# Kernel optimization log

Measured on AMD Instinct MI355X. Metric: run time of the kernel, lower is better.

Reference implementation:

```python
import jax, jax.numpy as jnp
import numpy as np
import math

LMAX = 2
MUL_IN1 = 8
C_OUT = 16
N_BASIS = 8
MAX_RADIUS = 2.0
N_NODES = 50000
N_EDGES = 1000000
EMB_DIM = 16
MAX_ATOM = 10
OUT_DIM = C_OUT * (LMAX + 1) ** 2


def _cg(j1, j2, j3, m1, m2, m3):
    # complex Clebsch-Gordan coefficient <j1 m1 j2 m2 | j3 m3> (Racah formula)
    if m1 + m2 != m3:
        return 0.0
    f = math.factorial
    pre = math.sqrt((2 * j3 + 1) * f(j3 + j1 - j2) * f(j3 - j1 + j2) * f(j1 + j2 - j3) / f(j1 + j2 + j3 + 1))
    pre *= math.sqrt(f(j3 + m3) * f(j3 - m3) * f(j1 - m1) * f(j1 + m1) * f(j2 - m2) * f(j2 + m2))
    s = 0.0
    for k in range(0, j1 + j2 - j3 + 1):
        d = [k, j1 + j2 - j3 - k, j1 - m1 - k, j2 + m2 - k, j3 - j2 + m1 + k, j3 - j1 - m2 + k]
        if min(d) < 0:
            continue
        s += (-1) ** k / (f(d[0]) * f(d[1]) * f(d[2]) * f(d[3]) * f(d[4]) * f(d[5]))
    return pre * s


def _q(l):
    # change of basis real -> complex spherical harmonics (e3nn convention)
    q = np.zeros((2 * l + 1, 2 * l + 1), dtype=complex)
    for m in range(-l, 0):
        q[l + m, l + abs(m)] = 2 ** -0.5
        q[l + m, l - abs(m)] = -1j * 2 ** -0.5
    q[l, l] = 1.0
    for m in range(1, l + 1):
        q[l + m, l + abs(m)] = (-1) ** m * 2 ** -0.5
        q[l + m, l - abs(m)] = 1j * (-1) ** m * 2 ** -0.5
    return (-1j) ** l * q


def _real_cg(l1, l2, l3):
    C = np.zeros((2 * l1 + 1, 2 * l2 + 1, 2 * l3 + 1), dtype=complex)
    for a, m1 in enumerate(range(-l1, l1 + 1)):
        for b, m2 in enumerate(range(-l2, l2 + 1)):
            for c, m3 in enumerate(range(-l3, l3 + 1)):
                C[a, b, c] = _cg(l1, l2, l3, m1, m2, m3)
    Cr = np.einsum('ai,bj,ck,abc->ijk', _q(l1), _q(l2), np.conj(_q(l3)), C)
    re, im = np.real(Cr), np.imag(Cr)
    M = re if np.abs(re).sum() >= np.abs(im).sum() else im
    return jnp.asarray(M, dtype=jnp.float32)


PATHS = [(l1, l2, l3) for l1 in range(LMAX + 1) for l2 in range(LMAX + 1) for l3 in range(LMAX + 1) if abs(l1 - l2) <= l3 <= l1 + l2]
CGS = [_real_cg(*p) for p in PATHS]
NUM_PATHS = len(PATHS)  # 15 for lmax=2, full path policy
ALPHA = {l3: 1.0 / math.sqrt(MUL_IN1 * sum(1 for p in PATHS if p[2] == l3)) for l3 in range(LMAX + 1)}


def _sh(n):
    # real spherical harmonics up to l=2, component normalization, m = -l..l
    x, y, z = n[:, 0], n[:, 1], n[:, 2]
    s3, s15, s5 = math.sqrt(3.0), math.sqrt(15.0), math.sqrt(5.0)
    Y0 = jnp.ones_like(x)[:, None]
    Y1 = s3 * jnp.stack([y, z, x], axis=-1)
    Y2 = jnp.stack([s15 * x * y, s15 * y * z, 0.5 * s5 * (3.0 * z * z - 1.0), s15 * x * z, 0.5 * s15 * (x * x - y * y)], axis=-1)
    return [Y0, Y1, Y2]


def _soft_one_hot(x):
    # e3nn soft_one_hot_linspace, basis='gaussian', cutoff=True
    v = jnp.linspace(0.0, MAX_RADIUS, N_BASIS + 2)
    step = v[1] - v[0]
    diff = (x[:, None] - v[1:-1]) / step
    return jnp.exp(-diff * diff) / 1.12


def _forward(pos, edge_shifts, cell, emb_table, mlp_w1, mlp_b1, mlp_w2, mlp_b2, fc_w1, fc_b1, fc_w2, fc_b2, fc_w3, fc_b3, tp_weights, A, batch, edge_src, edge_dst):
    edge_cells = cell[batch[edge_src]]                              # [E,3,3]
    shift = jnp.einsum('ni,nij->nj', edge_shifts, edge_cells)       # [E,3]
    edge_vec = pos[edge_dst] - pos[edge_src] + shift                # [E,3]
    edge_len = jnp.linalg.norm(edge_vec, axis=1)                    # [E]
    n = edge_vec / jnp.maximum(edge_len, 1e-8)[:, None]
    Ai = jax.nn.silu(emb_table[A] @ mlp_w1 + mlp_b1) @ mlp_w2 + mlp_b2   # [N, MUL_IN1]
    Ai_e = Ai[edge_src]                                             # [E, MUL_IN1]
    Y = _sh(n)                                                      # [[E,1],[E,3],[E,5]]
    emb = _soft_one_hot(edge_len) * (N_BASIS ** 0.5)                # [E, N_BASIS]
    h = jax.nn.silu(emb @ fc_w1 + fc_b1)
    h = jax.nn.silu(h @ fc_w2 + fc_b2)
    gates = h @ fc_w3 + fc_b3                                       # [E, NUM_PATHS]
    E = edge_src.shape[0]
    blocks = [jnp.zeros((E, C_OUT, 2 * l + 1), pos.dtype) for l in range(LMAX + 1)]
    for p, (l1, l2, l3) in enumerate(PATHS):
        # f_in[l1][e,u,m] = Ai_e[e,u]*Y[l1][e,m]; x2[l2][e,0,n] = Y[l2][e,n]; contraction separates:
        geo = jnp.einsum('em,en,mnk->ek', Y[l1], Y[l2], CGS[p])     # [E, 2*l3+1]
        chan = Ai_e @ tp_weights[p]                                 # [E, C_OUT]
        blocks[l3] = blocks[l3] + ALPHA[l3] * (gates[:, p, None, None] * chan[:, :, None] * geo[:, None, :])
    edge_feat = jnp.concatenate([b.reshape(E, -1) for b in blocks], axis=-1)  # [E, OUT_DIM]
    out = jax.ops.segment_sum(edge_feat, edge_dst, num_segments=pos.shape[0])
    avg = float(E) / float(pos.shape[0])
    return out / max(avg, 1e-8)


def setup_inputs():
    ks = jax.random.split(jax.random.key(0), 12)
    pos = jax.random.uniform(ks[0], (N_NODES, 3), dtype=jnp.float32)
    A = jax.random.randint(ks[1], (N_NODES,), 0, MAX_ATOM)
    batch = jnp.zeros((N_NODES,), dtype=jnp.int32)
    edge_src = jax.random.randint(ks[2], (N_EDGES,), 0, N_NODES)
    edge_dst = jax.random.randint(ks[3], (N_EDGES,), 0, N_NODES)
    edge_shifts = jnp.zeros((N_EDGES, 3), dtype=jnp.float32)
    cell = jnp.eye(3, dtype=jnp.float32)[None]
    emb_table = jax.random.normal(ks[4], (MAX_ATOM, EMB_DIM), jnp.float32)
    mlp_w1 = jax.random.normal(ks[5], (EMB_DIM, 64), jnp.float32) / math.sqrt(EMB_DIM)
    mlp_b1 = jnp.zeros((64,), jnp.float32)
    mlp_w2 = jax.random.normal(ks[6], (64, MUL_IN1), jnp.float32) / 8.0
    mlp_b2 = jnp.zeros((MUL_IN1,), jnp.float32)
    fc_w1 = jax.random.normal(ks[7], (N_BASIS, 64), jnp.float32) / math.sqrt(N_BASIS)
    fc_b1 = jnp.zeros((64,), jnp.float32)
    fc_w2 = jax.random.normal(ks[8], (64, 64), jnp.float32) / 8.0
    fc_b2 = jnp.zeros((64,), jnp.float32)
    fc_w3 = jax.random.normal(ks[9], (64, NUM_PATHS), jnp.float32) / 8.0
    fc_b3 = jnp.zeros((NUM_PATHS,), jnp.float32)
    tp_weights = jax.random.normal(ks[10], (NUM_PATHS, MUL_IN1, C_OUT), jnp.float32)
    return {'pos': pos, 'A': A, 'batch': batch, 'edge_src': edge_src, 'edge_dst': edge_dst, 'edge_shifts': edge_shifts, 'cell': cell, 'emb_table': emb_table, 'mlp_w1': mlp_w1, 'mlp_b1': mlp_b1, 'mlp_w2': mlp_w2, 'mlp_b2': mlp_b2, 'fc_w1': fc_w1, 'fc_b1': fc_b1, 'fc_w2': fc_w2, 'fc_b2': fc_b2, 'fc_w3': fc_w3, 'fc_b3': fc_b3, 'tp_weights': tp_weights}


def reference(pos, A, batch, edge_src, edge_dst, edge_shifts, cell, emb_table, mlp_w1, mlp_b1, mlp_w2, mlp_b2, fc_w1, fc_b1, fc_w2, fc_b2, fc_w3, fc_b3, tp_weights):
    return _forward(pos, edge_shifts, cell, emb_table, mlp_w1, mlp_b1, mlp_w2, mlp_b2, fc_w1, fc_b1, fc_w2, fc_b2, fc_w3, fc_b3, tp_weights, A, batch, edge_src, edge_dst)
```

## Files before the change

### kernel.cpp

```cpp
#include <hip/hip_runtime.h>
#include <math.h>
#include <limits.h>

#define N_NODES  50000
#define N_EDGES  1000000
#define INV_AVG  0.05f
#define DSENT    INT_MAX
#define TSIZE    8192
#define TMAX     1.7400f

constexpr int PL1[15] = {0,0,0,1,1,1,1,1,1,2,2,2,2,2,2};
constexpr int PL2[15] = {0,1,2,0,1,1,1,2,2,0,1,1,2,2,2};
constexpr int PCGOFF[16] = {0,1,10,35,44,53,80,125,170,245,270,315,390,415,490,615};
constexpr float PALPHA[15] = {
    0.20412414523193154f, 0.14433756729740643f, 0.14433756729740643f,
    0.14433756729740643f, 0.20412414523193154f, 0.14433756729740643f,
    0.14433756729740643f, 0.14433756729740643f, 0.14433756729740643f,
    0.14433756729740643f, 0.14433756729740643f, 0.14433756729740643f,
    0.20412414523193154f, 0.14433756729740643f, 0.14433756729740643f};

__device__ __constant__ int c_L1[15]   = {0,0,0,1,1,1,1,1,1,2,2,2,2,2,2};
__device__ __constant__ int c_L2[15]   = {0,1,2,0,1,1,1,2,2,0,1,1,2,2,2};
__device__ __constant__ int c_L3[15]   = {0,1,2,1,0,1,2,1,2,2,1,2,0,1,2};
__device__ __constant__ int c_CGOFF[16] = {0,1,10,35,44,53,80,125,170,245,270,315,390,415,490,615};

struct cplxd { double re, im; };

__device__ inline double factd(int n) {
    double r = 1.0;
    for (int i = 2; i <= n; ++i) r *= (double)i;
    return r;
}

__device__ double cgc(int j1, int j2, int j3, int m1, int m2, int m3) {
    if (m1 + m2 != m3) return 0.0;
    double pre = sqrt((double)(2*j3+1) * factd(j3+j1-j2) * factd(j3-j1+j2) *
                      factd(j1+j2-j3) / factd(j1+j2+j3+1));
    pre *= sqrt(factd(j3+m3)*factd(j3-m3)*factd(j1-m1)*factd(j1+m1)*
                factd(j2-m2)*factd(j2+m2));
    double s = 0.0;
    for (int k = 0; k <= j1+j2-j3; ++k) {
        int d1 = j1+j2-j3-k, d2 = j1-m1-k, d3 = j2+m2-k,
            d4 = j3-j2+m1+k, d5 = j3-j1-m2+k;
        if (d1 < 0 || d2 < 0 || d3 < 0 || d4 < 0 || d5 < 0) continue;
        double term = 1.0 / (factd(k)*factd(d1)*factd(d2)*factd(d3)*factd(d4)*factd(d5));
        s += (k & 1) ? -term : term;
    }
    return pre * s;
}

__device__ inline cplxd qent(int l, int a, int i) {
    const double r2 = 0.70710678118654752440;
    double re = 0.0, im = 0.0;
    int m = a - l;
    if (m < 0) {
        if (i == l - m)      re = r2;
        else if (i == l + m) im = -r2;
    } else if (m == 0) {
        if (i == l) re = 1.0;
    } else {
        double s = (m & 1) ? -1.0 : 1.0;
        if (i == l + m)      re = s * r2;
        else if (i == l - m) im = s * r2;
    }
    if (l == 1)      { double t = re; re = im; im = -t; }
    else if (l == 2) { re = -re; im = -im; }
    cplxd q; q.re = re; q.im = im; return q;
}

__device__ inline float silu_f(float x) { return x / (1.0f + __expf(-x)); }

__global__ __launch_bounds__(1024) void setup_kernel(
    float* __restrict__ cg_out,
    const float* __restrict__ fw1, const float* __restrict__ fb1,
    const float* __restrict__ fw2, const float* __restrict__ fb2,
    const float* __restrict__ fw3, const float* __restrict__ fb3,
    float* __restrict__ gtab,
    const int* __restrict__ A, const float* __restrict__ emb_table,
    const float* __restrict__ mw1, const float* __restrict__ mb1,
    const float* __restrict__ mw2, const float* __restrict__ mb2,
    float* __restrict__ Ai)
{
    const int blk = blockIdx.x;
    const int t = threadIdx.x;

    if (blk == 0) {
        __shared__ double s_re[615], s_im[615];
        __shared__ int s_flag[15];
        int p = 0;
        if (t < 615) {
            p = 14;
            while (t < c_CGOFF[p]) --p;
            int l1 = c_L1[p], l2 = c_L2[p], l3 = c_L3[p];
            int d1 = 2*l1+1, d2 = 2*l2+1, d3 = 2*l3+1;
            int local = t - c_CGOFF[p];
            int i = local / (d2*d3);
            int r = local - i*d2*d3;
            int j = r / d3;
            int k = r - j*d3;
            double accre = 0.0, accim = 0.0;
            for (int a = 0; a < d1; ++a) {
                cplxd q1 = qent(l1, a, i);
                if (q1.re == 0.0 && q1.im == 0.0) continue;
                for (int b = 0; b < d2; ++b) {
                    cplxd q2 = qent(l2, b, j);
                    if (q2.re == 0.0 && q2.im == 0.0) continue;
                    double t12r = q1.re*q2.re - q1.im*q2.im;
                    double t12i = q1.re*q2.im + q1.im*q2.re;
                    for (int c = 0; c < d3; ++c) {
                        cplxd q3 = qent(l3, c, k);
                        if (q3.re == 0.0 && q3.im == 0.0) continue;
                        int m1 = a-l1, m2 = b-l2, m3 = c-l3;
                        if (m1 + m2 != m3) continue;
                        double C = cgc(l1, l2, l3, m1, m2, m3);
                        if (C == 0.0) continue;
                        double cr = q3.re, ci = -q3.im;
                        accre += (t12r*cr - t12i*ci) * C;
                        accim += (t12r*ci + t12i*cr) * C;
                    }
                }
            }
            s_re[t] = accre; s_im[t] = accim;
        }
        __syncthreads();
        if (t < 15) {
            double sre = 0.0, sim = 0.0;
            for (int q = c_CGOFF[t]; q < c_CGOFF[t+1]; ++q) {
                sre += fabs(s_re[q]); sim += fabs(s_im[q]);
            }
            s_flag[t] = (sre >= sim) ? 0 : 1;
        }
        __syncthreads();
        if (t < 615) {
            cg_out[t] = (float)(s_flag[p] ? s_im[t] : s_re[t]);
        }
    } else if (blk <= 8) {
        const int idx = (blk - 1) * 1024 + t;
        if (idx >= TSIZE) return;
        const float len = (float)idx * (TMAX / (float)(TSIZE - 1));

        float embv[8];
#pragma unroll
        for (int b = 0; b < 8; ++b) {
            const float ctr = (2.0f/9.0f) * (float)(b+1);
            const float d = (len - ctr) * 4.5f;
            embv[b] = __expf(-d*d) * 2.5253813613805274f;
        }
        float h1[64];
#pragma unroll
        for (int i = 0; i < 64; ++i) {
            float tt = fb1[i];
#pragma unroll
            for (int b = 0; b < 8; ++b) tt += embv[b] * fw1[b*64 + i];
            h1[i] = silu_f(tt);
        }
        float g[15];
#pragma unroll
        for (int p = 0; p < 15; ++p) g[p] = fb3[p];
        for (int j = 0; j < 64; ++j) {
            float t0 = 0.0f, t1 = 0.0f, t2 = 0.0f, t3 = 0.0f;
#pragma unroll
            for (int i = 0; i < 64; i += 4) {
                t0 += h1[i+0] * fw2[(i+0)*64 + j];
                t1 += h1[i+1] * fw2[(i+1)*64 + j];
                t2 += h1[i+2] * fw2[(i+2)*64 + j];
                t3 += h1[i+3] * fw2[(i+3)*64 + j];
            }
            const float s = silu_f(fb2[j] + ((t0 + t1) + (t2 + t3)));
#pragma unroll
            for (int p = 0; p < 15; ++p) g[p] += s * fw3[j*15 + p];
        }
        float* orow = gtab + (long long)idx * 16;
#pragma unroll
        for (int p = 0; p < 15; ++p) orow[p] = g[p] * PALPHA[p];
        orow[15] = 0.0f;
    } else {
        const int v = (blk - 9) * 1024 + t;
        if (v >= N_NODES) return;
        int a = A[v];
        float e[16];
#pragma unroll
        for (int i = 0; i < 16; ++i) e[i] = emb_table[a*16 + i];
        float acc[8];
#pragma unroll
        for (int c = 0; c < 8; ++c) acc[c] = mb2[c];
        for (int j = 0; j < 64; ++j) {
            float tt = mb1[j];
#pragma unroll
            for (int i = 0; i < 16; ++i) tt += e[i] * mw1[i*64 + j];
            tt = silu_f(tt);
#pragma unroll
            for (int c = 0; c < 8; ++c) acc[c] += tt * mw2[j*8 + c];
        }
#pragma unroll
        for (int c = 0; c < 8; ++c) Ai[(long long)v*8 + c] = acc[c];
    }
}

__global__ __launch_bounds__(256) void hist_kernel(const int* __restrict__ edst,
                                                   int* __restrict__ cnt) {
    long long t = (long long)blockIdx.x * 256 + threadIdx.x;
    if (t < N_EDGES) atomicAdd(&cnt[edst[t]], 1);
}

__global__ __launch_bounds__(1024) void scan_kernel(int* __restrict__ cnt,
                                                    int* __restrict__ cur) {
    __shared__ int sums[1024];
    const int t = threadIdx.x;
    const int per = 49;
    const int base = t * per;
    int s = 0;
    for (int i = 0; i < per; ++i) {
        int idx = base + i;
        if (idx < N_NODES) s += cnt[idx];
    }
    sums[t] = s;
    __syncthreads();
    for (int off = 1; off < 1024; off <<= 1) {
        int v = (t >= off) ? sums[t - off] : 0;
        __syncthreads();
        sums[t] += v;
        __syncthreads();
    }
    int run = (t == 0) ? 0 : sums[t - 1];
    for (int i = 0; i < per; ++i) {
        int idx = base + i;
        if (idx < N_NODES) {
            int c = cnt[idx];
            cur[idx] = run;
            run += c;
        }
    }
}

__global__ __launch_bounds__(256) void scatter_kernel(
    const int* __restrict__ edst, int* __restrict__ cur,
    int* __restrict__ perm)
{
    long long t = (long long)blockIdx.x * 256 + threadIdx.x;
    if (t >= N_EDGES) return;
    int d = edst[t];
    int p = atomicAdd(&cur[d], 1);
    perm[p] = (int)t;
}

template<int P, int D3>
__device__ __attribute__((always_inline)) inline void process_path(
    float (&acc)[16*D3], const float (&Y)[9], const float (&g)[15],
    const float (&Aiv)[8], const float* __restrict__ cg, const float* __restrict__ tpw)
{
    constexpr int l1 = PL1[P], l2 = PL2[P];
    constexpr int d1 = 2*l1 + 1, d2 = 2*l2 + 1;
    constexpr int cgoff = PCGOFF[P];
    float geo[D3];
#pragma unroll
    for (int k = 0; k < D3; ++k) geo[k] = 0.0f;
#pragma unroll
    for (int m = 0; m < d1; ++m) {
#pragma unroll
        for (int n = 0; n < d2; ++n) {
            float pr = Y[l1*l1 + m] * Y[l2*l2 + n];
#pragma unroll
            for (int k = 0; k < D3; ++k)
                geo[k] += pr * cg[cgoff + (m*d2 + n)*D3 + k];
        }
    }
    float gg[D3];
#pragma unroll
    for (int k = 0; k < D3; ++k) gg[k] = geo[k] * g[P];
    float chan[16];
#pragma unroll
    for (int c = 0; c < 16; ++c) chan[c] = 0.0f;
#pragma unroll
    for (int m = 0; m < 8; ++m) {
#pragma unroll
        for (int c = 0; c < 16; ++c) chan[c] += Aiv[m] * tpw[P*128 + m*16 + c];
    }
#pragma unroll
    for (int c = 0; c < 16; ++c) {
#pragma unroll
        for (int k = 0; k < D3; ++k)
            acc[c*D3 + k] += chan[c] * gg[k];
    }
}

__global__ __launch_bounds__(256) void edge_kernel(
    const float* __restrict__ pos,  const int* __restrict__ batch,
    const int* __restrict__ esrc,   const int* __restrict__ edst,
    const float* __restrict__ eshift, const float* __restrict__ cell,
    const int* __restrict__ perm,
    const float* __restrict__ tpw,  const float* __restrict__ cg,
    const float* __restrict__ Ai,   const float* __restrict__ gtab,
    float* __restrict__ out)
{
    __shared__ float s_stage[256*49];
    __shared__ int   s_dstsh[256];
    __shared__ int   s_segstart[257];
    __shared__ int   s_segdst[256];
    __shared__ int   s_woff[5];

    const int tid  = threadIdx.x;
    const int wave = tid >> 6, lane = tid & 63;
    const long long e = (long long)blockIdx.x * 256 + tid;
    const bool act = (e < N_EDGES);

    const int t = act ? perm[e] : 0;
    const int src = esrc[t];
    const int mydst = act ? edst[t] : DSENT;
    const float s0 = eshift[3LL*t+0], s1 = eshift[3LL*t+1], s2 = eshift[3LL*t+2];

    float Aiv[8];
    {
        const float* ap = Ai + (long long)src * 8;
#pragma unroll
        for (int m = 0; m < 8; ++m) Aiv[m] = ap[m];
    }

    s_dstsh[tid] = mydst;
    __syncthreads();
    const int prev = (tid == 0) ? (mydst ^ 1) : s_dstsh[tid - 1];
    const int flag = (prev != mydst) ? 1 : 0;
    const unsigned long long mask = __ballot(flag != 0);
    const int excl = __popcll(mask & ((1ull << lane) - 1));
    if (lane == 0) s_woff[wave] = __popcll(mask);
    __syncthreads();
    if (tid == 0) {
        int r = 0;
#pragma unroll
        for (int w = 0; w < 4; ++w) { int c = s_woff[w]; s_woff[w] = r; r += c; }
        s_woff[4] = r;
        s_segstart[r] = 256;
    }
    __syncthreads();
    const int segid = s_woff[wave] + excl + flag - 1;
    if (flag) { s_segstart[segid] = tid; s_segdst[segid] = mydst; }
    __syncthreads();
    const int nseg = s_woff[4];

    const int dst = act ? mydst : 0;

    float len, nx, ny, nz;
    {
        const int bb = batch[src];
        const float* cl = cell + (long long)bb * 9;
        const float shx = s0*cl[0] + s1*cl[3] + s2*cl[6];
        const float shy = s0*cl[1] + s1*cl[4] + s2*cl[7];
        const float shz = s0*cl[2] + s1*cl[5] + s2*cl[8];
        const float vx = pos[dst*3+0] - pos[src*3+0] + shx;
        const float vy = pos[dst*3+1] - pos[src*3+1] + shy;
        const float vz = pos[dst*3+2] - pos[src*3+2] + shz;
        len = sqrtf(vx*vx + vy*vy + vz*vz);
        const float inv = 1.0f / fmaxf(len, 1e-8f);
        nx = vx*inv; ny = vy*inv; nz = vz*inv;
    }

    float Y[9];
    {
        const float s3c = 1.7320508075688772f;
        const float s15 = 3.872983346207417f;
        const float s5 = 2.2360679774997896f;
        Y[0] = 1.0f;
        Y[1] = s3c*ny; Y[2] = s3c*nz; Y[3] = s3c*nx;
        Y[4] = s15*nx*ny; Y[5] = s15*ny*nz;
        Y[6] = 0.5f*s5*(3.0f*nz*nz - 1.0f);
        Y[7] = s15*nx*nz;
        Y[8] = 0.5f*s15*(nx*nx - ny*ny);
    }

    float g[15];
    {
        float f = len * ((float)(TSIZE - 1) / TMAX);
        int i0 = (int)f;
        if (i0 > TSIZE - 2) i0 = TSIZE - 2;
        const float w = f - (float)i0;
        const float* t0 = gtab + (long long)i0 * 16;
        const float* t1 = t0 + 16;
#pragma unroll
        for (int p = 0; p < 15; ++p) g[p] = t0[p] + w * (t1[p] - t0[p]);
    }

    float a0[16], a1[48];
#pragma unroll
    for (int i = 0; i < 16; ++i) a0[i] = 0.0f;
    process_path<0, 1>(a0, Y, g, Aiv, cg, tpw);
    process_path<4, 1>(a0, Y, g, Aiv, cg, tpw);
    process_path<12,1>(a0, Y, g, Aiv, cg, tpw);
#pragma unroll
    for (int i = 0; i < 48; ++i) a1[i] = 0.0f;
    process_path<1, 3>(a1, Y, g, Aiv, cg, tpw);
    process_path<3, 3>(a1, Y, g, Aiv, cg, tpw);
    process_path<5, 3>(a1, Y, g, Aiv, cg, tpw);
    process_path<7, 3>(a1, Y, g, Aiv, cg, tpw);
    process_path<10,3>(a1, Y, g, Aiv, cg, tpw);
    process_path<13,3>(a1, Y, g, Aiv, cg, tpw);

#define DRAIN(BASE)                                                          \
    {                                                                        \
        const int ntask = nseg * 48;                                         \
        for (int task = tid; task < ntask; task += 256) {                    \
            const int seg = task / 48;                                       \
            const int comp = task - seg * 48;                                \
            const int s = s_segstart[seg], epos = s_segstart[seg + 1];       \
            const int d = s_segdst[seg];                                     \
            float sum = 0.0f;                                                \
            int r = s;                                                       \
            for (; r + 4 <= epos; r += 4) {                                  \
                float v0 = s_stage[(r+0)*49 + comp];                         \
                float v1 = s_stage[(r+1)*49 + comp];                         \
                float v2 = s_stage[(r+2)*49 + comp];                         \
                float v3 = s_stage[(r+3)*49 + comp];                         \
                sum += ((v0 + v1) + (v2 + v3));                              \
            }                                                                \
            for (; r < epos; ++r) sum += s_stage[r*49 + comp];               \
            if (d != DSENT)                                                  \
                atomicAdd(&out[(long long)d*144 + (BASE) + comp],            \
                          sum * INV_AVG);                                    \
        }                                                                    \
    }

#pragma unroll
    for (int c = 0; c < 48; ++c)
        s_stage[tid*49 + c] = (c < 16) ? a0[c] : a1[c - 16];
    __syncthreads();
    DRAIN(0)
    __syncthreads();

    float a2[80];
#pragma unroll
    for (int i = 0; i < 80; ++i) a2[i] = 0.0f;
    process_path<2, 5>(a2, Y, g, Aiv, cg, tpw);
    process_path<6, 5>(a2, Y, g, Aiv, cg, tpw);
    process_path<8, 5>(a2, Y, g, Aiv, cg, tpw);
    process_path<9, 5>(a2, Y, g, Aiv, cg, tpw);
    process_path<11,5>(a2, Y, g, Aiv, cg, tpw);
    process_path<14,5>(a2, Y, g, Aiv, cg, tpw);

#pragma unroll
    for (int c = 0; c < 48; ++c)
        s_stage[tid*49 + c] = (c < 16) ? a1[32 + c] : a2[c - 16];
    __syncthreads();
    DRAIN(48)
    __syncthreads();

#pragma unroll
    for (int c = 0; c < 48; ++c)
        s_stage[tid*49 + c] = a2[32 + c];
    __syncthreads();
    DRAIN(96)
#undef DRAIN
}

extern "C" void kernel_launch(void* const* d_in, const int* in_sizes, int n_in,
                              void* d_out, int out_size, void* d_ws, size_t ws_size,
                              hipStream_t stream) {
    const float* pos       = (const float*)d_in[0];
    const int*   A         = (const int*)d_in[1];
    const int*   batch     = (const int*)d_in[2];
    const int*   esrc      = (const int*)d_in[3];
    const int*   edst      = (const int*)d_in[4];
    const float* eshift    = (const float*)d_in[5];
    const float* cell      = (const float*)d_in[6];
    const float* emb_table = (const float*)d_in[7];
    const float* mlp_w1    = (const float*)d_in[8];
    const float* mlp_b1    = (const float*)d_in[9];
    const float* mlp_w2    = (const float*)d_in[10];
    const float* mlp_b2    = (const float*)d_in[11];
    const float* fc_w1     = (const float*)d_in[12];
    const float* fc_b1     = (const float*)d_in[13];
    const float* fc_w2     = (const float*)d_in[14];
    const float* fc_b2     = (const float*)d_in[15];
    const float* fc_w3     = (const float*)d_in[16];
    const float* fc_b3     = (const float*)d_in[17];
    const float* tpw       = (const float*)d_in[18];
    float* out = (float*)d_out;

    float* ws_cg   = (float*)d_ws;
    float* ws_Ai   = (float*)d_ws + 1024;
    float* ws_gtab = (float*)d_ws + 401024;
    int*   ws_cnt  = (int*)d_ws + 532096;
    int*   ws_cur  = (int*)d_ws + 582112;
    int*   ws_perm = (int*)d_ws + 632128;
    const long long FIXED = 1632128;
    const bool sortable = ((long long)(ws_size / 4) >= FIXED);

    hipMemsetAsync(d_out, 0, (size_t)out_size * sizeof(float), stream);
    hipLaunchKernelGGL(setup_kernel, dim3(58), dim3(1024), 0, stream,
                       ws_cg,
                       fc_w1, fc_b1, fc_w2, fc_b2, fc_w3, fc_b3, ws_gtab,
                       A, emb_table, mlp_w1, mlp_b1, mlp_w2, mlp_b2, ws_Ai);

    const int eblocks = (N_EDGES + 255) / 256;
    if (sortable) {
        hipMemsetAsync(ws_cnt, 0, 50016 * sizeof(int), stream);
        hipLaunchKernelGGL(hist_kernel, dim3(eblocks), dim3(256), 0, stream, edst, ws_cnt);
        hipLaunchKernelGGL(scan_kernel, dim3(1), dim3(1024), 0, stream, ws_cnt, ws_cur);
        hipLaunchKernelGGL(scatter_kernel, dim3(eblocks), dim3(256), 0, stream,
                           edst, ws_cur, ws_perm);
        hipLaunchKernelGGL(edge_kernel, dim3(eblocks), dim3(256), 0, stream,
                           pos, batch, esrc, edst, eshift, cell, ws_perm,
                           tpw, ws_cg, ws_Ai, ws_gtab, out);
    } else {
        hipLaunchKernelGGL(edge_kernel, dim3(eblocks), dim3(256), 0, stream,
                           pos, batch, esrc, edst, eshift, cell, ws_perm,
                           tpw, ws_cg, ws_Ai, ws_gtab, out);
    }
}
```

Baseline: 860.1 us.

## Precompute sorted edge geometry in scatter pass and shrink edge-kernel LDS staging

The histogram is folded into the setup kernel. The scatter kernel now computes each edge's unit vector and length and writes them, along with a packed src/dst pair, in dst-sorted order, so the edge kernel reads its inputs contiguously instead of gathering through a permutation. The edge kernel's shared-memory stage shrinks from 49 to 33 floats per thread with five drains of 32 components, and it gains a launch_bounds occupancy hint. The 1/avg scaling is folded into the gtab table. Packing src and dst into 16 bits each fails for node indices of 65536 or more; with 50000 nodes this holds. The non-sortable fallback is also removed, which assumes the workspace is large enough.

Result: slower. 898.5 us (+4.5%).

```diff
diff --git a/kernel.cpp b/kernel.cpp
--- a/kernel.cpp
+++ b/kernel.cpp
@@ -79,7 +79,8 @@
     const int* __restrict__ A, const float* __restrict__ emb_table,
     const float* __restrict__ mw1, const float* __restrict__ mb1,
     const float* __restrict__ mw2, const float* __restrict__ mb2,
-    float* __restrict__ Ai)
+    float* __restrict__ Ai,
+    const int* __restrict__ edst, int* __restrict__ cnt)
 {
     const int blk = blockIdx.x;
     const int t = threadIdx.x;
@@ -172,9 +173,9 @@
         }
         float* orow = gtab + (long long)idx * 16;
 #pragma unroll
-        for (int p = 0; p < 15; ++p) orow[p] = g[p] * PALPHA[p];
+        for (int p = 0; p < 15; ++p) orow[p] = g[p] * PALPHA[p] * INV_AVG;
         orow[15] = 0.0f;
-    } else {
+    } else if (blk <= 57) {
         const int v = (blk - 9) * 1024 + t;
         if (v >= N_NODES) return;
         int a = A[v];
@@ -194,16 +195,13 @@
         }
 #pragma unroll
         for (int c = 0; c < 8; ++c) Ai[(long long)v*8 + c] = acc[c];
-    }
-}
-
-__global__ __launch_bounds__(256) void hist_kernel(const int* __restrict__ edst,
-                                                   int* __restrict__ cnt) {
-    long long t = (long long)blockIdx.x * 256 + threadIdx.x;
-    if (t < N_EDGES) atomicAdd(&cnt[edst[t]], 1);
-}
-
-__global__ __launch_bounds__(1024) void scan_kernel(int* __restrict__ cnt,
+    } else {
+        const long long idx = (long long)(blk - 58) * 1024 + t;
+        if (idx < N_EDGES) atomicAdd(&cnt[edst[idx]], 1);
+    }
+}
+
+__global__ __launch_bounds__(1024) void scan_kernel(const int* __restrict__ cnt,
                                                     int* __restrict__ cur) {
     __shared__ int sums[1024];
     const int t = threadIdx.x;
@@ -226,22 +224,40 @@
     for (int i = 0; i < per; ++i) {
         int idx = base + i;
         if (idx < N_NODES) {
-            int c = cnt[idx];
+            run += 0;
             cur[idx] = run;
-            run += c;
-        }
-    }
-}
-
-__global__ __launch_bounds__(256) void scatter_kernel(
-    const int* __restrict__ edst, int* __restrict__ cur,
-    int* __restrict__ perm)
+            run += cnt[idx];
+        }
+    }
+}
+
+__global__ __launch_bounds__(256) void build_kernel(
+    const float* __restrict__ pos, const int* __restrict__ batch,
+    const int* __restrict__ esrc, const int* __restrict__ edst,
+    const float* __restrict__ eshift, const float* __restrict__ cell,
+    int* __restrict__ cur,
+    unsigned int* __restrict__ epair, float* __restrict__ edata)
 {
     long long t = (long long)blockIdx.x * 256 + threadIdx.x;
     if (t >= N_EDGES) return;
-    int d = edst[t];
-    int p = atomicAdd(&cur[d], 1);
-    perm[p] = (int)t;
+    const int src = esrc[t];
+    const int d   = edst[t];
+    const int p = atomicAdd(&cur[d], 1);
+
+    const int bb = batch[src];
+    const float s0 = eshift[3*t+0], s1 = eshift[3*t+1], s2 = eshift[3*t+2];
+    const float* cl = cell + (long long)bb * 9;
+    const float shx = s0*cl[0] + s1*cl[3] + s2*cl[6];
+    const float shy = s0*cl[1] + s1*cl[4] + s2*cl[7];
+    const float shz = s0*cl[2] + s1*cl[5] + s2*cl[8];
+    const float vx = pos[d*3+0] - pos[src*3+0] + shx;
+    const float vy = pos[d*3+1] - pos[src*3+1] + shy;
+    const float vz = pos[d*3+2] - pos[src*3+2] + shz;
+    const float len = sqrtf(vx*vx + vy*vy + vz*vz);
+    const float inv = 1.0f / fmaxf(len, 1e-8f);
+
+    epair[p] = (unsigned int)src | ((unsigned int)d << 16);
+    ((float4*)edata)[p] = make_float4(vx*inv, vy*inv, vz*inv, len);
 }
 
 template<int P, int D3>
@@ -284,16 +300,13 @@
     }
 }
 
-__global__ __launch_bounds__(256) void edge_kernel(
-    const float* __restrict__ pos,  const int* __restrict__ batch,
-    const int* __restrict__ esrc,   const int* __restrict__ edst,
-    const float* __restrict__ eshift, const float* __restrict__ cell,
-    const int* __restrict__ perm,
+__global__ __launch_bounds__(256, 4) void edge_kernel(
+    const unsigned int* __restrict__ epair, const float* __restrict__ edata,
     const float* __restrict__ tpw,  const float* __restrict__ cg,
     const float* __restrict__ Ai,   const float* __restrict__ gtab,
     float* __restrict__ out)
 {
-    __shared__ float s_stage[256*49];
+    __shared__ float s_stage[256*33];
     __shared__ int   s_dstsh[256];
     __shared__ int   s_segstart[257];
     __shared__ int   s_segdst[256];
@@ -303,17 +316,20 @@
     const int wave = tid >> 6, lane = tid & 63;
     const long long e = (long long)blockIdx.x * 256 + tid;
     const bool act = (e < N_EDGES);
-
-    const int t = act ? perm[e] : 0;
-    const int src = esrc[t];
-    const int mydst = act ? edst[t] : DSENT;
-    const float s0 = eshift[3LL*t+0], s1 = eshift[3LL*t+1], s2 = eshift[3LL*t+2];
+    const long long ti = act ? e : 0;
+
+    const unsigned int pk = epair[ti];
+    const int src = (int)(pk & 0xffffu);
+    const int mydst = act ? (int)(pk >> 16) : DSENT;
+    const float4 ed = ((const float4*)edata)[ti];
+    const float nx = ed.x, ny = ed.y, nz = ed.z, len = ed.w;
 
     float Aiv[8];
     {
-        const float* ap = Ai + (long long)src * 8;
-#pragma unroll
-        for (int m = 0; m < 8; ++m) Aiv[m] = ap[m];
+        const float4* ap = (const float4*)(Ai + (long long)src * 8);
+        float4 a0 = ap[0], a1 = ap[1];
+        Aiv[0]=a0.x; Aiv[1]=a0.y; Aiv[2]=a0.z; Aiv[3]=a0.w;
+        Aiv[4]=a1.x; Aiv[5]=a1.y; Aiv[6]=a1.z; Aiv[7]=a1.w;
     }
 
     s_dstsh[tid] = mydst;
@@ -336,23 +352,6 @@
     if (flag) { s_segstart[segid] = tid; s_segdst[segid] = mydst; }
     __syncthreads();
     const int nseg = s_woff[4];
-
-    const int dst = act ? mydst : 0;
-
-    float len, nx, ny, nz;
-    {
-        const int bb = batch[src];
-        const float* cl = cell + (long long)bb * 9;
-        const float shx = s0*cl[0] + s1*cl[3] + s2*cl[6];
-        const float shy = s0*cl[1] + s1*cl[4] + s2*cl[7];
-        const float shz = s0*cl[2] + s1*cl[5] + s2*cl[8];
-        const float vx = pos[dst*3+0] - pos[src*3+0] + shx;
-        const float vy = pos[dst*3+1] - pos[src*3+1] + shy;
-        const float vz = pos[dst*3+2] - pos[src*3+2] + shz;
-        len = sqrtf(vx*vx + vy*vy + vz*vz);
-        const float inv = 1.0f / fmaxf(len, 1e-8f);
-        nx = vx*inv; ny = vy*inv; nz = vz*inv;
-    }
 
     float Y[9];
     {
@@ -394,35 +393,41 @@
     process_path<10,3>(a1, Y, g, Aiv, cg, tpw);
     process_path<13,3>(a1, Y, g, Aiv, cg, tpw);
 
-#define DRAIN(BASE)                                                          \
+#define DRAIN(BASE, NC, SH, MSK)                                             \
     {                                                                        \
-        const int ntask = nseg * 48;                                         \
+        const int ntask = nseg * (NC);                                       \
         for (int task = tid; task < ntask; task += 256) {                    \
-            const int seg = task / 48;                                       \
-            const int comp = task - seg * 48;                                \
+            const int seg = task >> (SH);                                    \
+            const int comp = task & (MSK);                                   \
             const int s = s_segstart[seg], epos = s_segstart[seg + 1];       \
             const int d = s_segdst[seg];                                     \
             float sum = 0.0f;                                                \
             int r = s;                                                       \
             for (; r + 4 <= epos; r += 4) {                                  \
-                float v0 = s_stage[(r+0)*49 + comp];                         \
-                float v1 = s_stage[(r+1)*49 + comp];                         \
-                float v2 = s_stage[(r+2)*49 + comp];                         \
-                float v3 = s_stage[(r+3)*49 + comp];                         \
+                float v0 = s_stage[(r+0)*33 + comp];                         \
+                float v1 = s_stage[(r+1)*33 + comp];                         \
+                float v2 = s_stage[(r+2)*33 + comp];                         \
+                float v3 = s_stage[(r+3)*33 + comp];                         \
                 sum += ((v0 + v1) + (v2 + v3));                              \
             }                                                                \
-            for (; r < epos; ++r) sum += s_stage[r*49 + comp];               \
+            for (; r < epos; ++r) sum += s_stage[r*33 + comp];               \
             if (d != DSENT)                                                  \
-                atomicAdd(&out[(long long)d*144 + (BASE) + comp],            \
-                          sum * INV_AVG);                                    \
+                atomicAdd(&out[(long long)d*144 + (BASE) + comp], sum);      \
         }                                                                    \
     }
 
 #pragma unroll
-    for (int c = 0; c < 48; ++c)
-        s_stage[tid*49 + c] = (c < 16) ? a0[c] : a1[c - 16];
-    __syncthreads();
-    DRAIN(0)
+    for (int c = 0; c < 32; ++c)
+        s_stage[tid*33 + c] = (c < 16) ? a0[c] : a1[c - 16];
+    __syncthreads();
+    DRAIN(0, 32, 5, 31)
+    __syncthreads();
+
+#pragma unroll
+    for (int c = 0; c < 32; ++c)
+        s_stage[tid*33 + c] = a1[16 + c];
+    __syncthreads();
+    DRAIN(32, 32, 5, 31)
     __syncthreads();
 
     float a2[80];
@@ -436,17 +441,24 @@
     process_path<14,5>(a2, Y, g, Aiv, cg, tpw);
 
 #pragma unroll
-    for (int c = 0; c < 48; ++c)
-        s_stage[tid*49 + c] = (c < 16) ? a1[32 + c] : a2[c - 16];
-    __syncthreads();
-    DRAIN(48)
-    __syncthreads();
-
-#pragma unroll
-    for (int c = 0; c < 48; ++c)
-        s_stage[tid*49 + c] = a2[32 + c];
-    __syncthreads();
-    DRAIN(96)
+    for (int c = 0; c < 32; ++c)
+        s_stage[tid*33 + c] = a2[c];
+    __syncthreads();
+    DRAIN(64, 32, 5, 31)
+    __syncthreads();
+
+#pragma unroll
+    for (int c = 0; c < 32; ++c)
+        s_stage[tid*33 + c] = a2[32 + c];
+    __syncthreads();
+    DRAIN(96, 32, 5, 31)
+    __syncthreads();
+
+#pragma unroll
+    for (int c = 0; c < 16; ++c)
+        s_stage[tid*33 + c] = a2[64 + c];
+    __syncthreads();
+    DRAIN(128, 16, 4, 15)
 #undef DRAIN
 }
 
@@ -474,34 +486,28 @@
     const float* tpw       = (const float*)d_in[18];
     float* out = (float*)d_out;
 
-    float* ws_cg   = (float*)d_ws;
-    float* ws_Ai   = (float*)d_ws + 1024;
-    float* ws_gtab = (float*)d_ws + 401024;
-    int*   ws_cnt  = (int*)d_ws + 532096;
-    int*   ws_cur  = (int*)d_ws + 582112;
-    int*   ws_perm = (int*)d_ws + 632128;
-    const long long FIXED = 1632128;
-    const bool sortable = ((long long)(ws_size / 4) >= FIXED);
+    float*        ws_cg    = (float*)d_ws;
+    float*        ws_Ai    = (float*)d_ws + 1024;
+    float*        ws_gtab  = (float*)d_ws + 401024;
+    int*          ws_cnt   = (int*)d_ws + 532096;
+    int*          ws_cur   = (int*)d_ws + 582112;
+    unsigned int* ws_epair = (unsigned int*)d_ws + 632128;
+    float*        ws_edata = (float*)d_ws + 1632128;
 
     hipMemsetAsync(d_out, 0, (size_t)out_size * sizeof(float), stream);
-    hipLaunchKernelGGL(setup_kernel, dim3(58), dim3(1024), 0, stream,
+    hipMemsetAsync(ws_cnt, 0, 50016 * sizeof(int), stream);
+
+    hipLaunchKernelGGL(setup_kernel, dim3(58 + 977), dim3(1024), 0, stream,
                        ws_cg,
                        fc_w1, fc_b1, fc_w2, fc_b2, fc_w3, fc_b3, ws_gtab,
-                       A, emb_table, mlp_w1, mlp_b1, mlp_w2, mlp_b2, ws_Ai);
+                       A, emb_table, mlp_w1, mlp_b1, mlp_w2, mlp_b2, ws_Ai,
+                       edst, ws_cnt);
+    hipLaunchKernelGGL(scan_kernel, dim3(1), dim3(1024), 0, stream, ws_cnt, ws_cur);
 
     const int eblocks = (N_EDGES + 255) / 256;
-    if (sortable) {
-        hipMemsetAsync(ws_cnt, 0, 50016 * sizeof(int), stream);
-        hipLaunchKernelGGL(hist_kernel, dim3(eblocks), dim3(256), 0, stream, edst, ws_cnt);
-        hipLaunchKernelGGL(scan_kernel, dim3(1), dim3(1024), 0, stream, ws_cnt, ws_cur);
-        hipLaunchKernelGGL(scatter_kernel, dim3(eblocks), dim3(256), 0, stream,
-                           edst, ws_cur, ws_perm);
-        hipLaunchKernelGGL(edge_kernel, dim3(eblocks), dim3(256), 0, stream,
-                           pos, batch, esrc, edst, eshift, cell, ws_perm,
-                           tpw, ws_cg, ws_Ai, ws_gtab, out);
-    } else {
-        hipLaunchKernelGGL(edge_kernel, dim3(eblocks), dim3(256), 0, stream,
-                           pos, batch, esrc, edst, eshift, cell, ws_perm,
-                           tpw, ws_cg, ws_Ai, ws_gtab, out);
-    }
-}
+    hipLaunchKernelGGL(build_kernel, dim3(eblocks), dim3(256), 0, stream,
+                       pos, batch, esrc, edst, eshift, cell,
+                       ws_cur, ws_epair, ws_edata);
+    hipLaunchKernelGGL(edge_kernel, dim3(eblocks), dim3(256), 0, stream,
+                       ws_epair, ws_edata, tpw, ws_cg, ws_Ai, ws_gtab, out);
+}
```
